# Performance work log

Measured on AMD Instinct MI355X. Metric: run time of the kernel, lower is better.

The kernel has to match this reference:

```python
import jax, jax.numpy as jnp
import numpy as np

N_NODES = 50000
N_EDGES = 800000
C = 96           # num_channels = 3 ops + 2 acts + 89 hidden + 2
HID = 32         # update MLP hidden width


def setup_inputs() -> dict:
    key = jax.random.key(0)
    ks = jax.random.split(key, 7)
    x = jax.random.normal(ks[0], (N_NODES, C), dtype=jnp.float32)
    edge_index = jax.random.randint(ks[1], (2, N_EDGES), 0, N_NODES, dtype=jnp.int64)
    # GCNConv weight (no bias): in=C, out=3C
    W_gcn = jax.random.normal(ks[2], (C, 3 * C), dtype=jnp.float32) / np.sqrt(C)
    # update_net: Linear(3C, 32) -> ReLU -> Linear(32, C)
    W1 = jax.random.normal(ks[3], (3 * C, HID), dtype=jnp.float32) / np.sqrt(3 * C)
    b1 = jnp.zeros((HID,), dtype=jnp.float32)
    W2 = jax.random.normal(ks[4], (HID, C), dtype=jnp.float32) / np.sqrt(HID)
    b2 = jnp.zeros((C,), dtype=jnp.float32)
    return {"x": x, "W_gcn": W_gcn, "W1": W1, "b1": b1, "W2": W2, "b2": b2,
            "edge_index": edge_index}


def _gcn_conv(x, W, edge_index, n_nodes):
    # PyG GCNConv defaults: add self-loops, symmetric normalization, no bias.
    src, dst = edge_index[0], edge_index[1]
    loop = jnp.arange(n_nodes, dtype=src.dtype)
    src = jnp.concatenate([src, loop])
    dst = jnp.concatenate([dst, loop])
    deg = jax.ops.segment_sum(jnp.ones_like(dst, dtype=x.dtype), dst,
                              num_segments=n_nodes)
    dinv = jnp.where(deg > 0, jax.lax.rsqrt(deg), 0.0)
    norm = dinv[src] * dinv[dst]                      # [E+N]
    h = x @ W                                         # [N, 3C] project first (cheaper)
    msg = h[src] * norm[:, None]                      # gather + scale  [E+N, 3C]
    return jax.ops.segment_sum(msg, dst, num_segments=n_nodes)  # scatter-add [N, 3C]


def reference(x, W_gcn, W1, b1, W2, b2, edge_index):
    n_nodes = x.shape[0]
    features = _gcn_conv(x, W_gcn, edge_index, n_nodes)          # perception_net
    update = jax.nn.relu(features @ W1 + b1) @ W2 + b2           # update_net
    return x + update                                            # residual
```

## Files before the change

### kernel.cpp

```cpp
#include <hip/hip_runtime.h>
#include <hip/hip_bf16.h>

#define N_NODES 50000
#define N_EDGES 800000
#define C 96
#define C3 288
#define HID 32
#define GPB 8
#define BSH 7
#define NBUCK 391
#define E4 (N_EDGES / 4)
#define CBLK 391


__global__ void k_wf(const float* __restrict__ Wg, const float* __restrict__ W1,
                     float* __restrict__ Wf, int* __restrict__ gbhist) {
    int kt = blockIdx.x * 256 + threadIdx.x;
    if (kt < NBUCK) gbhist[kt] = 0;
    if (kt >= C * HID) return;
    int k = kt >> 5, j = kt & 31;
    float acc = 0.f;
    for (int m = 0; m < C3; ++m)
        acc += Wg[k * C3 + m] * W1[m * HID + j];
    Wf[k * HID + j] = acc;
}


__global__ __launch_bounds__(512) void kA(const int* __restrict__ dst,
                                          int* __restrict__ gbhist) {
    __shared__ int h[NBUCK];
    const int t = threadIdx.x;
    for (int i = t; i < NBUCK; i += 512) h[i] = 0;
    __syncthreads();
    int e4 = blockIdx.x * 512 + t;
    if (e4 < E4) {
        int4 d = ((const int4*)dst)[e4];
        atomicAdd(&h[d.x >> BSH], 1);
        atomicAdd(&h[d.y >> BSH], 1);
        atomicAdd(&h[d.z >> BSH], 1);
        atomicAdd(&h[d.w >> BSH], 1);
    }
    __syncthreads();
    for (int i = t; i < NBUCK; i += 512)
        if (h[i]) atomicAdd(&gbhist[i], h[i]);
}


__global__ __launch_bounds__(512) void kB(const int* __restrict__ gbhist,
                                          int* __restrict__ bucket_base,
                                          int* __restrict__ bucket_cursor,
                                          int* __restrict__ rowstart) {
    __shared__ int s[512];
    const int t = threadIdx.x;
    int v = (t < NBUCK) ? gbhist[t] : 0;
    s[t] = v;
    __syncthreads();
    for (int off = 1; off < 512; off <<= 1) {
        int a = (t >= off) ? s[t - off] : 0;
        __syncthreads();
        s[t] += a;
        __syncthreads();
    }
    if (t < NBUCK) { int ex = s[t] - v; bucket_base[t] = ex; bucket_cursor[t] = ex; }
    if (t == 0) { bucket_base[NBUCK] = N_EDGES; rowstart[N_NODES] = N_EDGES; }
}


__global__ __launch_bounds__(512) void kC(const int* __restrict__ src,
                                          const int* __restrict__ dst,
                                          int* __restrict__ bucket_cursor,
                                          unsigned int* __restrict__ packed) {
    __shared__ int h[NBUCK];
    __shared__ int pre[NBUCK];
    __shared__ int runbase[NBUCK];
    __shared__ int lcur[NBUCK];
    __shared__ int s[512];
    __shared__ unsigned int staged[2048];
    __shared__ unsigned short sb[2048];
    const int t = threadIdx.x;
    for (int i = t; i < NBUCK; i += 512) h[i] = 0;
    __syncthreads();

    const int e4 = blockIdx.x * 512 + t;
    const bool valid = e4 < E4;
    int4 sv, dv;
    if (valid) {
        sv = ((const int4*)src)[e4];
        dv = ((const int4*)dst)[e4];
        atomicAdd(&h[dv.x >> BSH], 1);
        atomicAdd(&h[dv.y >> BSH], 1);
        atomicAdd(&h[dv.z >> BSH], 1);
        atomicAdd(&h[dv.w >> BSH], 1);
    }
    __syncthreads();

    int v = (t < NBUCK) ? h[t] : 0;
    s[t] = v;
    __syncthreads();
    for (int off = 1; off < 512; off <<= 1) {
        int a = (t >= off) ? s[t - off] : 0;
        __syncthreads();
        s[t] += a;
        __syncthreads();
    }
    if (t < NBUCK) {
        int ex = s[t] - v;
        pre[t] = ex;
        lcur[t] = ex;
        if (v) runbase[t] = atomicAdd(&bucket_cursor[t], v);
    }
    __syncthreads();

    if (valid) {
        int b0 = dv.x >> BSH, p0 = atomicAdd(&lcur[b0], 1);
        staged[p0] = (unsigned)sv.x | ((unsigned)(dv.x & 127) << 16); sb[p0] = (unsigned short)b0;
        int b1 = dv.y >> BSH, p1 = atomicAdd(&lcur[b1], 1);
        staged[p1] = (unsigned)sv.y | ((unsigned)(dv.y & 127) << 16); sb[p1] = (unsigned short)b1;
        int b2 = dv.z >> BSH, p2 = atomicAdd(&lcur[b2], 1);
        staged[p2] = (unsigned)sv.z | ((unsigned)(dv.z & 127) << 16); sb[p2] = (unsigned short)b2;
        int b3 = dv.w >> BSH, p3 = atomicAdd(&lcur[b3], 1);
        staged[p3] = (unsigned)sv.w | ((unsigned)(dv.w & 127) << 16); sb[p3] = (unsigned short)b3;
    }
    __syncthreads();

    int cntT = N_EDGES - blockIdx.x * 2048;
    if (cntT > 2048) cntT = 2048;
    for (int i = t; i < cntT; i += 512) {
        int b = sb[i];
        packed[runbase[b] + (i - pre[b])] = staged[i];
    }
}


__global__ __launch_bounds__(256) void kD(const int* __restrict__ bucket_base,
                                          const unsigned int* __restrict__ packed,
                                          int* __restrict__ rowstart,
                                          int* __restrict__ srcs) {
    __shared__ int cnt[128], pre2[128], cur[128];
    const int b = blockIdx.x, t = threadIdx.x;
    const int base = bucket_base[b];
    const int cnt_e = bucket_base[b + 1] - base;
    if (t < 128) cnt[t] = 0;
    __syncthreads();
    for (int i = t; i < cnt_e; i += 256)
        atomicAdd(&cnt[(packed[base + i] >> 16) & 127], 1);
    __syncthreads();
    int v = (t < 128) ? cnt[t] : 0;
    if (t < 128) pre2[t] = v;
    __syncthreads();
    for (int off = 1; off < 128; off <<= 1) {
        int a = (t < 128 && t >= off) ? pre2[t - off] : 0;
        __syncthreads();
        if (t < 128) pre2[t] += a;
        __syncthreads();
    }
    const int node = b * 128 + t;
    if (t < 128) {
        int ex = pre2[t] - v;
        cur[t] = ex;
        if (node < N_NODES) rowstart[node] = base + ex;
    }
    __syncthreads();
    for (int i = t; i < cnt_e; i += 256) {
        unsigned p = packed[base + i];
        int pos = atomicAdd(&cur[(p >> 16) & 127], 1);
        srcs[base + pos] = (int)(p & 0xFFFFu);
    }
}


__global__ __launch_bounds__(256) void k_z(
        const float* __restrict__ x, const int* __restrict__ rowstart,
        const float* __restrict__ Wf, __hip_bfloat16* __restrict__ z) {
    __shared__ float xs[GPB][C];
    const int t = threadIdx.x, l = t & 31, grp = t >> 5;
    const int g = blockIdx.x * GPB + grp;
    const float di = rsqrtf((float)(rowstart[g + 1] - rowstart[g] + 1));
    const float* xr = x + (size_t)g * C;
    xs[grp][l]      = xr[l]      * di;
    xs[grp][l + 32] = xr[l + 32] * di;
    xs[grp][l + 64] = xr[l + 64] * di;
    float acc = 0.f;
    #pragma unroll 8
    for (int k = 0; k < C; ++k)
        acc = fmaf(xs[grp][k], Wf[k * HID + l], acc);
    z[(size_t)g * HID + l] = __float2bfloat16(acc);
}


__global__ __launch_bounds__(256) void k_fused(
        const int* __restrict__ rowstart, const int* __restrict__ srcs,
        const __hip_bfloat16* __restrict__ z, const float* __restrict__ x,
        const float* __restrict__ b1, const float* __restrict__ W2,
        const float* __restrict__ b2, float* __restrict__ out) {
    const int t = threadIdx.x, l = t & 31;
    const int g = blockIdx.x * GPB + (t >> 5);
    const int rs = rowstart[g], re = rowstart[g + 1];
    const float di = rsqrtf((float)(re - rs + 1));

    float h = __bfloat162float(z[(size_t)g * HID + l]);
    int e = rs;
    for (; e + 8 <= re; e += 8) {
        int s0 = srcs[e],     s1 = srcs[e + 1], s2 = srcs[e + 2], s3 = srcs[e + 3];
        int s4 = srcs[e + 4], s5 = srcs[e + 5], s6 = srcs[e + 6], s7 = srcs[e + 7];
        float v0 = __bfloat162float(z[(size_t)s0 * HID + l]);
        float v1 = __bfloat162float(z[(size_t)s1 * HID + l]);
        float v2 = __bfloat162float(z[(size_t)s2 * HID + l]);
        float v3 = __bfloat162float(z[(size_t)s3 * HID + l]);
        float v4 = __bfloat162float(z[(size_t)s4 * HID + l]);
        float v5 = __bfloat162float(z[(size_t)s5 * HID + l]);
        float v6 = __bfloat162float(z[(size_t)s6 * HID + l]);
        float v7 = __bfloat162float(z[(size_t)s7 * HID + l]);
        h += ((v0 + v1) + (v2 + v3)) + ((v4 + v5) + (v6 + v7));
    }
    for (; e + 2 <= re; e += 2) {
        int s0 = srcs[e], s1 = srcs[e + 1];
        h += __bfloat162float(z[(size_t)s0 * HID + l])
           + __bfloat162float(z[(size_t)s1 * HID + l]);
    }
    if (e < re) h += __bfloat162float(z[(size_t)srcs[e] * HID + l]);

    const float hid = fmaxf(fmaf(h, di, b1[l]), 0.f);

    float o0 = b2[l], o1 = b2[l + 32], o2 = b2[l + 64];
    const int base = t & 32;
    #pragma unroll
    for (int hh = 0; hh < HID; ++hh) {
        float hv = __shfl(hid, base + hh, 64);
        o0 = fmaf(hv, W2[hh * C + l],      o0);
        o1 = fmaf(hv, W2[hh * C + l + 32], o1);
        o2 = fmaf(hv, W2[hh * C + l + 64], o2);
    }
    const float* xr = x + (size_t)g * C;
    float* orow = out + (size_t)g * C;
    orow[l]      = xr[l]      + o0;
    orow[l + 32] = xr[l + 32] + o1;
    orow[l + 64] = xr[l + 64] + o2;
}


extern "C" void kernel_launch(void* const* d_in, const int* in_sizes, int n_in,
                              void* d_out, int out_size, void* d_ws, size_t ws_size,
                              hipStream_t stream) {
    const float* x   = (const float*)d_in[0];
    const float* Wg  = (const float*)d_in[1];
    const float* W1  = (const float*)d_in[2];
    const float* b1  = (const float*)d_in[3];
    const float* W2  = (const float*)d_in[4];
    const float* b2  = (const float*)d_in[5];
    const int* ei  = (const int*)d_in[6];
    const int* src = ei;
    const int* dst = ei + N_EDGES;
    float* out = (float*)d_out;

    char* w = (char*)d_ws;
    int* gbhist        = (int*)w;             w += NBUCK * 4;
    int* bucket_base   = (int*)w;             w += (NBUCK + 1) * 4;
    int* bucket_cursor = (int*)w;             w += NBUCK * 4;
    int* rowstart      = (int*)w;             w += (N_NODES + 1) * 4;
    unsigned int* packed = (unsigned int*)w;  w += N_EDGES * 4;
    int* srcs          = (int*)w;             w += N_EDGES * 4;
    float* Wf          = (float*)w;           w += C * HID * 4;
    __hip_bfloat16* z  = (__hip_bfloat16*)w;

    k_wf   <<<(C * HID + 255) / 256, 256, 0, stream>>>(Wg, W1, Wf, gbhist);
    kA     <<<CBLK, 512, 0, stream>>>(dst, gbhist);
    kB     <<<1,    512, 0, stream>>>(gbhist, bucket_base, bucket_cursor, rowstart);
    kC     <<<CBLK, 512, 0, stream>>>(src, dst, bucket_cursor, packed);
    kD     <<<NBUCK, 256, 0, stream>>>(bucket_base, packed, rowstart, srcs);
    k_z    <<<N_NODES / GPB, 256, 0, stream>>>(x, rowstart, Wf, z);
    k_fused<<<N_NODES / GPB, 256, 0, stream>>>(rowstart, srcs, z, x, b1, W2, b2, out);
}
```

Baseline: 177.5 us.

## Pack bf16 pairs and process four nodes per half-wave in z and fused kernels

```diff
diff --git a/kernel.cpp b/kernel.cpp
--- a/kernel.cpp
+++ b/kernel.cpp
@@ -6,18 +6,26 @@
 #define C 96
 #define C3 288
 #define HID 32
-#define GPB 8
 #define BSH 7
 #define NBUCK 391
 #define E4 (N_EDGES / 4)
 #define CBLK 391
-
-
-__global__ void k_wf(const float* __restrict__ Wg, const float* __restrict__ W1,
-                     float* __restrict__ Wf, int* __restrict__ gbhist) {
-    int kt = blockIdx.x * 256 + threadIdx.x;
+#define ZPB 32
+#define FGPB 32
+#define NZB 1563
+
+__device__ __forceinline__ unsigned bf16_rne(float v) {
+    unsigned u = __float_as_uint(v);
+    return (u + 0x7FFFu + ((u >> 16) & 1u)) >> 16;
+}
+
+
+__global__ __launch_bounds__(64) void k_wf(const float* __restrict__ Wg,
+                                           const float* __restrict__ W1,
+                                           float* __restrict__ Wf,
+                                           int* __restrict__ gbhist) {
+    int kt = blockIdx.x * 64 + threadIdx.x;
     if (kt < NBUCK) gbhist[kt] = 0;
-    if (kt >= C * HID) return;
     int k = kt >> 5, j = kt & 31;
     float acc = 0.f;
     for (int m = 0; m < C3; ++m)
@@ -171,71 +179,156 @@
 
 __global__ __launch_bounds__(256) void k_z(
         const float* __restrict__ x, const int* __restrict__ rowstart,
-        const float* __restrict__ Wf, __hip_bfloat16* __restrict__ z) {
-    __shared__ float xs[GPB][C];
-    const int t = threadIdx.x, l = t & 31, grp = t >> 5;
-    const int g = blockIdx.x * GPB + grp;
-    const float di = rsqrtf((float)(rowstart[g + 1] - rowstart[g] + 1));
-    const float* xr = x + (size_t)g * C;
-    xs[grp][l]      = xr[l]      * di;
-    xs[grp][l + 32] = xr[l + 32] * di;
-    xs[grp][l + 64] = xr[l + 64] * di;
-    float acc = 0.f;
-    #pragma unroll 8
-    for (int k = 0; k < C; ++k)
-        acc = fmaf(xs[grp][k], Wf[k * HID + l], acc);
-    z[(size_t)g * HID + l] = __float2bfloat16(acc);
+        const float* __restrict__ Wf, unsigned int* __restrict__ zu) {
+    __shared__ float xs[ZPB * C];
+    const int t = threadIdx.x;
+    const int gbase = blockIdx.x * ZPB;
+    {
+        const float4* xsrc = (const float4*)(x + (size_t)gbase * C);
+        int nrem = N_NODES - gbase;
+        int nflt4 = ((nrem >= ZPB) ? ZPB * C : nrem * C) >> 2;
+        float4* xd = (float4*)xs;
+        for (int i = t; i < ZPB * C / 4; i += 256)
+            xd[i] = (i < nflt4) ? xsrc[i] : float4{0.f, 0.f, 0.f, 0.f};
+    }
+    __syncthreads();
+    const int l = t & 31, hw = t >> 5;
+    const float* xrow = xs + (hw * 4) * C;
+    float a0 = 0.f, a1 = 0.f, a2 = 0.f, a3 = 0.f;
+    #pragma unroll 4
+    for (int k = 0; k < C; ++k) {
+        float wf = Wf[k * HID + l];
+        a0 = fmaf(xrow[k],         wf, a0);
+        a1 = fmaf(xrow[C + k],     wf, a1);
+        a2 = fmaf(xrow[2 * C + k], wf, a2);
+        a3 = fmaf(xrow[3 * C + k], wf, a3);
+    }
+    const int g0 = gbase + hw * 4;
+    float acc[4] = {a0, a1, a2, a3};
+    #pragma unroll
+    for (int i = 0; i < 4; ++i) {
+        int g = g0 + i;
+        if (g < N_NODES) {
+            float di = rsqrtf((float)(rowstart[g + 1] - rowstart[g] + 1));
+            float zv = acc[i] * di;
+            unsigned mybits = bf16_rne(zv);
+            unsigned nbr = __shfl_down(mybits, 1, 32);
+            if ((l & 1) == 0)
+                zu[(size_t)g * 16 + (l >> 1)] = mybits | (nbr << 16);
+        }
+    }
 }
 
 
 __global__ __launch_bounds__(256) void k_fused(
         const int* __restrict__ rowstart, const int* __restrict__ srcs,
-        const __hip_bfloat16* __restrict__ z, const float* __restrict__ x,
+        const unsigned int* __restrict__ zu, const float* __restrict__ x,
         const float* __restrict__ b1, const float* __restrict__ W2,
         const float* __restrict__ b2, float* __restrict__ out) {
-    const int t = threadIdx.x, l = t & 31;
-    const int g = blockIdx.x * GPB + (t >> 5);
-    const int rs = rowstart[g], re = rowstart[g + 1];
-    const float di = rsqrtf((float)(re - rs + 1));
-
-    float h = __bfloat162float(z[(size_t)g * HID + l]);
-    int e = rs;
-    for (; e + 8 <= re; e += 8) {
-        int s0 = srcs[e],     s1 = srcs[e + 1], s2 = srcs[e + 2], s3 = srcs[e + 3];
-        int s4 = srcs[e + 4], s5 = srcs[e + 5], s6 = srcs[e + 6], s7 = srcs[e + 7];
-        float v0 = __bfloat162float(z[(size_t)s0 * HID + l]);
-        float v1 = __bfloat162float(z[(size_t)s1 * HID + l]);
-        float v2 = __bfloat162float(z[(size_t)s2 * HID + l]);
-        float v3 = __bfloat162float(z[(size_t)s3 * HID + l]);
-        float v4 = __bfloat162float(z[(size_t)s4 * HID + l]);
-        float v5 = __bfloat162float(z[(size_t)s5 * HID + l]);
-        float v6 = __bfloat162float(z[(size_t)s6 * HID + l]);
-        float v7 = __bfloat162float(z[(size_t)s7 * HID + l]);
-        h += ((v0 + v1) + (v2 + v3)) + ((v4 + v5) + (v6 + v7));
-    }
-    for (; e + 2 <= re; e += 2) {
-        int s0 = srcs[e], s1 = srcs[e + 1];
-        h += __bfloat162float(z[(size_t)s0 * HID + l])
-           + __bfloat162float(z[(size_t)s1 * HID + l]);
-    }
-    if (e < re) h += __bfloat162float(z[(size_t)srcs[e] * HID + l]);
-
-    const float hid = fmaxf(fmaf(h, di, b1[l]), 0.f);
-
-    float o0 = b2[l], o1 = b2[l + 32], o2 = b2[l + 64];
-    const int base = t & 32;
+    const int t = threadIdx.x, l = t & 31, hw = t >> 5;
+    const int sub = l >> 4, c2 = l & 15;
+    const int g0 = blockIdx.x * FGPB + hw * 4;
+
+    float hx[4] = {0.f, 0.f, 0.f, 0.f};
+    float hy[4] = {0.f, 0.f, 0.f, 0.f};
+    int   dg[4] = {1, 1, 1, 1};
+
     #pragma unroll
+    for (int i = 0; i < 4; ++i) {
+        int g = g0 + i;
+        if (g >= N_NODES) continue;
+        int rs = rowstart[g], re = rowstart[g + 1];
+        dg[i] = re - rs + 1;
+        float ax = 0.f, ay = 0.f;
+        if (sub == 0) {
+            unsigned zz = zu[(size_t)g * 16 + c2];
+            ax = __uint_as_float(zz << 16);
+            ay = __uint_as_float(zz & 0xFFFF0000u);
+        }
+        int e = rs;
+        while (e < re) {
+            int nb = re - e; if (nb > 32) nb = 32;
+            int myidx = 0;
+            if (l < nb) myidx = srcs[e + l];
+            int npair = nb >> 1, k = 0;
+            for (; k + 4 <= npair; k += 4) {
+                int s0 = __shfl(myidx, ((k + 0) << 1) | sub, 32);
+                int s1 = __shfl(myidx, ((k + 1) << 1) | sub, 32);
+                int s2 = __shfl(myidx, ((k + 2) << 1) | sub, 32);
+                int s3 = __shfl(myidx, ((k + 3) << 1) | sub, 32);
+                unsigned z0 = zu[(size_t)s0 * 16 + c2];
+                unsigned z1 = zu[(size_t)s1 * 16 + c2];
+                unsigned z2 = zu[(size_t)s2 * 16 + c2];
+                unsigned z3 = zu[(size_t)s3 * 16 + c2];
+                ax += (__uint_as_float(z0 << 16) + __uint_as_float(z1 << 16))
+                    + (__uint_as_float(z2 << 16) + __uint_as_float(z3 << 16));
+                ay += (__uint_as_float(z0 & 0xFFFF0000u) + __uint_as_float(z1 & 0xFFFF0000u))
+                    + (__uint_as_float(z2 & 0xFFFF0000u) + __uint_as_float(z3 & 0xFFFF0000u));
+            }
+            for (; k < npair; ++k) {
+                int s = __shfl(myidx, (k << 1) | sub, 32);
+                unsigned zz = zu[(size_t)s * 16 + c2];
+                ax += __uint_as_float(zz << 16);
+                ay += __uint_as_float(zz & 0xFFFF0000u);
+            }
+            if (nb & 1) {
+                int s = __shfl(myidx, nb - 1, 32);
+                if (sub == 0) {
+                    unsigned zz = zu[(size_t)s * 16 + c2];
+                    ax += __uint_as_float(zz << 16);
+                    ay += __uint_as_float(zz & 0xFFFF0000u);
+                }
+            }
+            e += nb;
+        }
+        hx[i] = ax; hy[i] = ay;
+    }
+
+    float hid[4];
+    const float bb1 = b1[l];
+    #pragma unroll
+    for (int i = 0; i < 4; ++i) {
+        float sx = hx[i] + __shfl_xor(hx[i], 16, 32);
+        float sy = hy[i] + __shfl_xor(hy[i], 16, 32);
+        float ex = __shfl(sx, l >> 1, 32);
+        float ey = __shfl(sy, l >> 1, 32);
+        float hch = (l & 1) ? ey : ex;
+        float di = rsqrtf((float)dg[i]);
+        hid[i] = fmaxf(fmaf(hch, di, bb1), 0.f);
+    }
+
+    const bool act = (l < 24);
+    float4 o0, o1, o2, o3;
+    {
+        float4 bb = act ? ((const float4*)b2)[l] : float4{0.f, 0.f, 0.f, 0.f};
+        o0 = bb; o1 = bb; o2 = bb; o3 = bb;
+    }
     for (int hh = 0; hh < HID; ++hh) {
-        float hv = __shfl(hid, base + hh, 64);
-        o0 = fmaf(hv, W2[hh * C + l],      o0);
-        o1 = fmaf(hv, W2[hh * C + l + 32], o1);
-        o2 = fmaf(hv, W2[hh * C + l + 64], o2);
-    }
-    const float* xr = x + (size_t)g * C;
-    float* orow = out + (size_t)g * C;
-    orow[l]      = xr[l]      + o0;
-    orow[l + 32] = xr[l + 32] + o1;
-    orow[l + 64] = xr[l + 64] + o2;
+        float4 w4 = act ? ((const float4*)(W2 + hh * C))[l] : float4{0.f, 0.f, 0.f, 0.f};
+        float hv0 = __shfl(hid[0], hh, 32);
+        float hv1 = __shfl(hid[1], hh, 32);
+        float hv2 = __shfl(hid[2], hh, 32);
+        float hv3 = __shfl(hid[3], hh, 32);
+        o0.x = fmaf(hv0, w4.x, o0.x); o0.y = fmaf(hv0, w4.y, o0.y);
+        o0.z = fmaf(hv0, w4.z, o0.z); o0.w = fmaf(hv0, w4.w, o0.w);
+        o1.x = fmaf(hv1, w4.x, o1.x); o1.y = fmaf(hv1, w4.y, o1.y);
+        o1.z = fmaf(hv1, w4.z, o1.z); o1.w = fmaf(hv1, w4.w, o1.w);
+        o2.x = fmaf(hv2, w4.x, o2.x); o2.y = fmaf(hv2, w4.y, o2.y);
+        o2.z = fmaf(hv2, w4.z, o2.z); o2.w = fmaf(hv2, w4.w, o2.w);
+        o3.x = fmaf(hv3, w4.x, o3.x); o3.y = fmaf(hv3, w4.y, o3.y);
+        o3.z = fmaf(hv3, w4.z, o3.z); o3.w = fmaf(hv3, w4.w, o3.w);
+    }
+
+    float4 oo[4] = {o0, o1, o2, o3};
+    #pragma unroll
+    for (int i = 0; i < 4; ++i) {
+        int g = g0 + i;
+        if (g < N_NODES && act) {
+            float4 xv = ((const float4*)(x + (size_t)g * C))[l];
+            float4 ov = {xv.x + oo[i].x, xv.y + oo[i].y, xv.z + oo[i].z, xv.w + oo[i].w};
+            ((float4*)(out + (size_t)g * C))[l] = ov;
+        }
+    }
 }
 
 
@@ -261,13 +354,13 @@
     unsigned int* packed = (unsigned int*)w;  w += N_EDGES * 4;
     int* srcs          = (int*)w;             w += N_EDGES * 4;
     float* Wf          = (float*)w;           w += C * HID * 4;
-    __hip_bfloat16* z  = (__hip_bfloat16*)w;
-
-    k_wf   <<<(C * HID + 255) / 256, 256, 0, stream>>>(Wg, W1, Wf, gbhist);
+    unsigned int* zu   = (unsigned int*)w;
+
+    k_wf   <<<48,    64, 0, stream>>>(Wg, W1, Wf, gbhist);
     kA     <<<CBLK, 512, 0, stream>>>(dst, gbhist);
     kB     <<<1,    512, 0, stream>>>(gbhist, bucket_base, bucket_cursor, rowstart);
     kC     <<<CBLK, 512, 0, stream>>>(src, dst, bucket_cursor, packed);
     kD     <<<NBUCK, 256, 0, stream>>>(bucket_base, packed, rowstart, srcs);
-    k_z    <<<N_NODES / GPB, 256, 0, stream>>>(x, rowstart, Wf, z);
-    k_fused<<<N_NODES / GPB, 256, 0, stream>>>(rowstart, srcs, z, x, b1, W2, b2, out);
-}
+    k_z    <<<NZB,  256, 0, stream>>>(x, rowstart, Wf, zu);
+    k_fused<<<NZB,  256, 0, stream>>>(rowstart, srcs, zu, x, b1, W2, b2, out);
+}
```

New measurement: 235.3 us. 32.6% more time.
